# Optimization experiments

Measured on AMD Instinct MI355X. Metric: run time of the kernel, lower is better.

The kernel has to match this reference:

```python
import jax, jax.numpy as jnp
import numpy as np

B, T, N, D, H, NMASK = 8192, 2, 40, 64, 1, 3
EPS = 1e-5


def setup_inputs() -> dict:
    key = jax.random.key(0)
    ks = jax.random.split(key, 12)
    F = T * N * 2 * D  # flattened feature size fed to BatchNorm1d
    return {
        "x": jax.random.normal(ks[0], (B, N, D), jnp.float32),
        "masker": jax.random.uniform(ks[1], (T, NMASK, N, N), jnp.float32, -0.27, 0.27),  # xavier-like
        "ln_gamma": jnp.ones((N,), jnp.float32),
        "ln_beta": jnp.zeros((N,), jnp.float32),
        "gnn_w": jax.random.normal(ks[2], (1, T, H, 2 * D, D), jnp.float32) * 0.05,
        "gnn_b": jax.random.normal(ks[3], (T, H, N, D), jnp.float32) * 0.05,
        "bn_gamma": jnp.ones((H, F), jnp.float32),
        "bn_beta": jnp.zeros((H, F), jnp.float32),
        "bn_mean": jax.random.normal(ks[4], (H, F), jnp.float32) * 0.1,
        "bn_var": jax.random.uniform(ks[5], (H, F), jnp.float32, 0.5, 1.5),
        "gate_w": jax.random.normal(ks[6], (N * D, N), jnp.float32) * 0.02,
        "gate_b": jnp.zeros((N,), jnp.float32),
    }


def reference(x, masker, ln_gamma, ln_beta, gnn_w, gnn_b, bn_gamma, bn_beta, bn_mean, bn_var, gate_w, gate_b):
    b = x.shape[0]
    # broadcast input to towers: (B, T, N, D)
    h = jnp.broadcast_to(x[:, None], (b, T, N, D))
    # adjacency from product of mask matrices: (T, N, N)
    adj = jax.nn.relu(jnp.prod(masker, axis=1))
    mask = (adj != 0).astype(x.dtype)
    # LayerNorm(num_fields) applied on transposed adj == normalize over rows (axis -2)
    mu = adj.mean(axis=-2, keepdims=True)
    var = adj.var(axis=-2, keepdims=True)
    ln = (adj - mu) / jnp.sqrt(var + EPS) * ln_gamma[:, None] + ln_beta[:, None]
    x_masked = ln + (1.0 - mask) * (-1e9) + jnp.eye(N, dtype=x.dtype)
    # softmax over rows (dim=1 of (T,N,N)) then re-mask
    A = jax.nn.softmax(x_masked, axis=1) * mask  # (T, N, N)
    for idx in range(H):
        # nei[b,t,n,d] = sum_m h[b,t,m,d] * A[t,m,n]
        nei = jnp.einsum('btmd,tmn->btnd', h, A)
        hc = jnp.concatenate([h, nei], axis=-1)  # (B,T,N,2D)
        flat = hc.reshape(b, -1)
        flat = (flat - bn_mean[idx]) / jnp.sqrt(bn_var[idx] + EPS) * bn_gamma[idx] + bn_beta[idx]
        hc = flat.reshape(b, T, N, 2 * D)
        # per-tower transform: (B,T,N,2D) x (T,2D,D) -> (B,T,N,D)
        h = jnp.einsum('btnf,tfd->btnd', hc, gnn_w[0, :, idx]) + gnn_b[:, idx]
    # attention pooling over fields
    logits = h.reshape(b, T, N * D) @ gate_w + gate_b  # (B,T,N)
    w = jax.nn.softmax(logits, axis=2)
    return jnp.sum(h * w[..., None], axis=2)  # (B, T, D)
```

## Files before the change

### kernel.cpp

```cpp
#include <hip/hip_runtime.h>
#include <hip/hip_bf16.h>
#include <stdint.h>

typedef float v4f __attribute__((ext_vector_type(4)));
typedef short v8s __attribute__((ext_vector_type(8)));

#define NB 40

__device__ __forceinline__ unsigned short f2b(float f) {
  __hip_bfloat16 h = __float2bfloat16(f);
  unsigned short u;
  __builtin_memcpy(&u, &h, 2);
  return u;
}
__device__ __forceinline__ unsigned pk2(float lo, float hi) {
  __hip_bfloat162 h = __float22bfloat162_rn(make_float2(lo, hi));
  unsigned u;
  __builtin_memcpy(&u, &h, 4);
  return u;
}
__device__ __forceinline__ float b2f16(unsigned short h) {
  return __uint_as_float(((unsigned)h) << 16);
}
__device__ __forceinline__ float blo(unsigned u) { return __uint_as_float(u << 16); }
__device__ __forceinline__ float bhi(unsigned u) { return __uint_as_float(u & 0xFFFF0000u); }


__global__ __launch_bounds__(256) void prep(
    const float* __restrict__ x, const float* __restrict__ masker,
    const float* __restrict__ ln_gamma, const float* __restrict__ ln_beta,
    const float* __restrict__ gnn_w, const float* __restrict__ gnn_b,
    const float* __restrict__ bn_gamma, const float* __restrict__ bn_beta,
    const float* __restrict__ bn_mean, const float* __restrict__ bn_var,
    const float* __restrict__ gate_w,
    unsigned short* __restrict__ A1pk, unsigned short* __restrict__ W2pk,
    unsigned short* __restrict__ Gpk, float* __restrict__ s1,
    float* __restrict__ sNT, float* __restrict__ bias2T,
    unsigned short* __restrict__ xk, unsigned short* __restrict__ xb16)
{
  __shared__ float AtL[2 * NB * NB];
  const int tid = threadIdx.x;

  {
    const int lane = tid & 63, bq = tid >> 6;
    const int b = blockIdx.x * 4 + bq;
    const float* xb = x + (size_t)b * 2560 + lane;
    unsigned u[20];
    #pragma unroll
    for (int mp = 0; mp < 20; ++mp)
      u[mp] = pk2(xb[(2*mp)*64], xb[(2*mp+1)*64]);
    unsigned short* dst = xk + ((size_t)b * 64 + lane) * 40;
    #pragma unroll
    for (int i = 0; i < 5; ++i)
      *(uint4*)(dst + i*8) = make_uint4(u[4*i], u[4*i+1], u[4*i+2], u[4*i+3]);
    const float4* xs4 = (const float4*)(x + (size_t)blockIdx.x * 10240);
    uint2* xd2 = (uint2*)(xb16 + (size_t)blockIdx.x * 10240);
    #pragma unroll
    for (int it = 0; it < 10; ++it) {
      float4 v = xs4[it*256 + tid];
      xd2[it*256 + tid] = make_uint2(pk2(v.x, v.y), pk2(v.z, v.w));
    }
  }

  if (blockIdx.x < 40) {
    const int gid = blockIdx.x * 256 + tid, gsz = 40 * 256;
    for (int e = gid; e < 16384; e += gsz) {
      int frag = e >> 9, rem = e & 511, lane = rem >> 3, jj = rem & 7;
      int t = frag >> 4, ks = (frag >> 2) & 3, dt = frag & 3;
      int f = ks*32 + (lane >> 4)*8 + jj, d = dt*16 + (lane & 15);
      W2pk[e] = f2b(gnn_w[t*8192 + f*64 + d]);
    }
    for (int e = gid; e < 122880; e += gsz) {
      int frag = e >> 9, rem = e & 511, lane = rem >> 3, jj = rem & 7;
      int kt = frag / 3, jt = frag % 3;
      int fl = kt*32 + (lane >> 4)*8 + jj, j = jt*16 + (lane & 15);
      Gpk[e] = f2b(j < NB ? gate_w[fl*NB + j] : 0.f);
    }
    for (int e = gid; e < 5120; e += gsz) {
      int t = e / 2560, n = (e % 2560) / 64, d = e & 63;
      int F = (t*NB + n)*128 + d;
      s1[e] = bn_gamma[F] * rsqrtf(bn_var[F] + 1e-5f);
    }
    for (int e = gid; e < 5120; e += gsz) {
      int t = e / 2560, d = (e % 2560) / 40, n = e % 40;
      int F = (t*NB + n)*128 + 64 + d;
      sNT[e] = bn_gamma[F] * rsqrtf(bn_var[F] + 1e-5f);
    }
    for (int e = gid; e < 5120; e += gsz) {
      int t = e / 2560, d = (e % 2560) / 40, n = e % 40;
      float acc = gnn_b[(t*NB + n)*64 + d];
      int Fb = (t*NB + n)*128;
      for (int f = 0; f < 128; ++f) {
        float s = bn_gamma[Fb+f] * rsqrtf(bn_var[Fb+f] + 1e-5f);
        float o = bn_beta[Fb+f] - bn_mean[Fb+f] * s;
        acc += o * gnn_w[t*8192 + f*64 + d];
      }
      bias2T[e] = acc;
    }
  } else if (blockIdx.x == 40) {
    for (int col = tid; col < 2 * NB; col += 256) {
      int t = col / NB, n = col % NB;
      float adj[NB];
      for (int m = 0; m < NB; ++m) {
        float p = masker[((t*3+0)*NB+m)*NB+n]
                * masker[((t*3+1)*NB+m)*NB+n]
                * masker[((t*3+2)*NB+m)*NB+n];
        adj[m] = p > 0.f ? p : 0.f;
      }
      float mu = 0.f;
      for (int m = 0; m < NB; ++m) mu += adj[m];
      mu *= (1.f/NB);
      float var = 0.f;
      for (int m = 0; m < NB; ++m) { float dv = adj[m]-mu; var += dv*dv; }
      var *= (1.f/NB);
      float inv = rsqrtf(var + 1e-5f);
      float xm[NB]; float mx = -3e38f;
      for (int m = 0; m < NB; ++m) {
        float lnv = (adj[m]-mu)*inv*ln_gamma[m] + ln_beta[m];
        float v = lnv + (adj[m] != 0.f ? 0.f : -1e9f) + (m==n ? 1.f : 0.f);
        xm[m] = v; mx = fmaxf(mx, v);
      }
      float ssum = 0.f;
      for (int m = 0; m < NB; ++m) { xm[m] = __expf(xm[m]-mx); ssum += xm[m]; }
      float isum = 1.f/ssum;
      for (int m = 0; m < NB; ++m)
        AtL[(t*NB+n)*NB+m] = (adj[m] != 0.f) ? xm[m]*isum : 0.f;
    }
    __syncthreads();
    for (int e = tid; e < 6144; e += 256) {
      int frag = e >> 9, rem = e & 511, lane = rem >> 3, jj = rem & 7;
      int t = frag / 6, r2 = frag % 6, nt = r2 >> 1, ks = r2 & 1;
      int n = nt*16 + (lane & 15);
      int m = ks*32 + (lane >> 4)*8 + jj;
      A1pk[e] = f2b((n < NB && m < NB) ? AtL[(t*NB+n)*NB+m] : 0.f);
    }
  }
}

__global__ __launch_bounds__(256) void kernelM(
    const unsigned short* __restrict__ xb16, const unsigned short* __restrict__ xk,
    const unsigned short* __restrict__ A1pk, const unsigned short* __restrict__ W2pk,
    const unsigned short* __restrict__ Gpk, const float* __restrict__ s1,
    const float* __restrict__ sNT, const float* __restrict__ bias2T,
    const float* __restrict__ gate_b, float* __restrict__ out)
{
  __shared__ __align__(16) unsigned short hc[160 * 136];
  __shared__ __align__(16) unsigned short hL[4 * 2568];
  __shared__ float pj[16 * 48];
  __shared__ float wgt[4 * NB];

  const int tid = threadIdx.x;
  const int lane = tid & 63;
  const int w = tid >> 6;
  const int l = lane & 15, q = lane >> 4;
  const int b0 = blockIdx.x * 4;
  unsigned* hcU = (unsigned*)hc;

  v8s b1[4][2];
  #pragma unroll
  for (int i = 0; i < 4; ++i)
    #pragma unroll
    for (int ks = 0; ks < 2; ++ks)
      b1[i][ks] = *(const v8s*)(xk + ((size_t)b0*64 + (w*4+i)*16 + l)*40 + ks*32 + q*8);
  v8s a1[2][3][2];
  #pragma unroll
  for (int t = 0; t < 2; ++t)
    #pragma unroll
    for (int nt = 0; nt < 3; ++nt)
      #pragma unroll
      for (int ks = 0; ks < 2; ++ks)
        a1[t][nt][ks] = *(const v8s*)(A1pk + (((t*3+nt)*2+ks) << 9) + lane*8);
  v8s w2[2][4];
  #pragma unroll
  for (int t = 0; t < 2; ++t)
    #pragma unroll
    for (int ks = 0; ks < 4; ++ks)
      w2[t][ks] = *(const v8s*)(W2pk + (((t*4+ks)*4 + w) << 9) + lane*8);

  uint4 xr[5];

  #pragma unroll
  for (int t = 0; t < 2; ++t) {
    #pragma unroll
    for (int it = 0; it < 5; ++it) {
      const int c = it*256 + tid;
      const int row = c >> 3, dp8 = c & 7;
      if (t == 0)
        xr[it] = *(const uint4*)((const unsigned*)xb16 + (size_t)b0*1280 + row*32 + dp8*4);
      const uint4 xv = xr[it];
      const int n = row % NB;
      const float4 sA = *(const float4*)(s1 + (t*NB + n)*64 + dp8*8);
      const float4 sB = *(const float4*)(s1 + (t*NB + n)*64 + dp8*8 + 4);
      uint4 p;
      p.x = pk2(blo(xv.x)*sA.x, bhi(xv.x)*sA.y);
      p.y = pk2(blo(xv.y)*sA.z, bhi(xv.y)*sA.w);
      p.z = pk2(blo(xv.z)*sB.x, bhi(xv.z)*sB.y);
      p.w = pk2(blo(xv.w)*sB.z, bhi(xv.w)*sB.w);
      *(uint4*)(hcU + row*68 + dp8*4) = p;
    }
    #pragma unroll
    for (int i = 0; i < 4; ++i) {
      const int R = (w*4+i)*16 + l;
      const int bb = R >> 6, d = R & 63;
      #pragma unroll
      for (int nt = 0; nt < 3; ++nt) {
        v4f acc = {0.f, 0.f, 0.f, 0.f};
        acc = __builtin_amdgcn_mfma_f32_16x16x32_bf16(a1[t][nt][0], b1[i][0], acc, 0, 0, 0);
        acc = __builtin_amdgcn_mfma_f32_16x16x32_bf16(a1[t][nt][1], b1[i][1], acc, 0, 0, 0);
        const float4 sv = *(const float4*)(sNT + (t*64+d)*40 + nt*16 + q*4);
        #pragma unroll
        for (int r = 0; r < 4; ++r) {
          int n = nt*16 + q*4 + r;
          if (n < NB) hc[(bb*NB + n)*136 + 64 + d] = f2b(acc[r]*sv[r]);
        }
      }
    }
    __syncthreads();
    #pragma unroll
    for (int mt = 0; mt < 10; ++mt) {
      v4f acc = {0.f, 0.f, 0.f, 0.f};
      #pragma unroll
      for (int ks = 0; ks < 4; ++ks) {
        v8s af = *(const v8s*)(hc + (mt*16 + l)*136 + ks*32 + q*8);
        acc = __builtin_amdgcn_mfma_f32_16x16x32_bf16(af, w2[t][ks], acc, 0, 0, 0);
      }
      const int d = w*16 + l;
      const int G = mt*16 + q*4;
      const int bb = G / NB, n0 = G - bb*NB;
      const float4 bv = *(const float4*)(bias2T + (t*64+d)*40 + n0);
      #pragma unroll
      for (int r = 0; r < 4; ++r)
        hL[bb*2568 + (n0+r)*64 + d] = f2b(acc[r] + bv[r]);
    }
    __syncthreads();
    v4f ac0 = {0,0,0,0}, ac1 = {0,0,0,0}, ac2 = {0,0,0,0};
    for (int kt = w; kt < 80; kt += 4) {
      v8s bf = *(const v8s*)(hL + (l & 3)*2568 + kt*32 + q*8);
      v8s g0 = *(const v8s*)(Gpk + ((kt*3+0) << 9) + lane*8);
      v8s g1 = *(const v8s*)(Gpk + ((kt*3+1) << 9) + lane*8);
      v8s g2 = *(const v8s*)(Gpk + ((kt*3+2) << 9) + lane*8);
      ac0 = __builtin_amdgcn_mfma_f32_16x16x32_bf16(g0, bf, ac0, 0, 0, 0);
      ac1 = __builtin_amdgcn_mfma_f32_16x16x32_bf16(g1, bf, ac1, 0, 0, 0);
      ac2 = __builtin_amdgcn_mfma_f32_16x16x32_bf16(g2, bf, ac2, 0, 0, 0);
    }
    if (l < 4) {
      #pragma unroll
      for (int r = 0; r < 4; ++r) {
        pj[(w*4 + l)*48 +  0 + q*4 + r] = ac0[r];
        pj[(w*4 + l)*48 + 16 + q*4 + r] = ac1[r];
        pj[(w*4 + l)*48 + 32 + q*4 + r] = ac2[r];
      }
    }
    __syncthreads();
    if (tid < 32) {
      const int bb = tid >> 3, s = tid & 7;
      float lv[5]; float mx = -3e38f;
      #pragma unroll
      for (int i = 0; i < 5; ++i) {
        int j = s*5 + i;
        float v = gate_b[j];
        #pragma unroll
        for (int ww = 0; ww < 4; ++ww) v += pj[(ww*4 + bb)*48 + j];
        lv[i] = v; mx = fmaxf(mx, v);
      }
      #pragma unroll
      for (int m = 1; m < 8; m <<= 1) mx = fmaxf(mx, __shfl_xor(mx, m));
      float es = 0.f;
      #pragma unroll
      for (int i = 0; i < 5; ++i) { lv[i] = __expf(lv[i] - mx); es += lv[i]; }
      #pragma unroll
      for (int m = 1; m < 8; m <<= 1) es += __shfl_xor(es, m);
      float inv = 1.f / es;
      #pragma unroll
      for (int i = 0; i < 5; ++i) wgt[bb*NB + s*5 + i] = lv[i]*inv;
    }
    __syncthreads();
    {
      float accp = 0.f;
      #pragma unroll 8
      for (int n = 0; n < NB; ++n)
        accp += b2f16(hL[w*2568 + n*64 + lane]) * wgt[w*NB + n];
      out[((size_t)(b0 + w)*2 + t)*64 + lane] = accp;
    }
  }
}

extern "C" void kernel_launch(void* const* d_in, const int* in_sizes, int n_in,
                              void* d_out, int out_size, void* d_ws, size_t ws_size,
                              hipStream_t stream) {
  const float* x        = (const float*)d_in[0];
  const float* masker   = (const float*)d_in[1];
  const float* ln_gamma = (const float*)d_in[2];
  const float* ln_beta  = (const float*)d_in[3];
  const float* gnn_w    = (const float*)d_in[4];
  const float* gnn_b    = (const float*)d_in[5];
  const float* bn_gamma = (const float*)d_in[6];
  const float* bn_beta  = (const float*)d_in[7];
  const float* bn_mean  = (const float*)d_in[8];
  const float* bn_var   = (const float*)d_in[9];
  const float* gate_w   = (const float*)d_in[10];
  const float* gate_b   = (const float*)d_in[11];
  float* out = (float*)d_out;

  char* ws = (char*)d_ws;
  unsigned short* A1pk   = (unsigned short*)(ws + 0);
  unsigned short* W2pk   = (unsigned short*)(ws + 12288);
  unsigned short* Gpk    = (unsigned short*)(ws + 45056);
  float*          s1     = (float*)(ws + 290816);
  float*          sNT    = (float*)(ws + 311296);
  float*          bias2T = (float*)(ws + 331904);
  unsigned short* xk     = (unsigned short*)(ws + 352384);
  unsigned short* xb16   = (unsigned short*)(ws + 42295552);

  prep<<<2048, 256, 0, stream>>>(x, masker, ln_gamma, ln_beta, gnn_w, gnn_b,
                                 bn_gamma, bn_beta, bn_mean, bn_var, gate_w,
                                 A1pk, W2pk, Gpk, s1, sNT, bias2T, xk, xb16);
  kernelM<<<2048, 256, 0, stream>>>(xb16, xk, A1pk, W2pk, Gpk,
                                    s1, sNT, bias2T, gate_b, out);
}
```

Baseline: 264.9 us.

## Offload bias folding to dedicated prep blocks and halve per-block batch in main kernel

After: 346.2 us. +30.7%, slower.

```diff
diff --git a/kernel.cpp b/kernel.cpp
--- a/kernel.cpp
+++ b/kernel.cpp
@@ -38,10 +38,13 @@
     float* __restrict__ sNT, float* __restrict__ bias2T,
     unsigned short* __restrict__ xk, unsigned short* __restrict__ xb16)
 {
-  __shared__ float AtL[2 * NB * NB];
+  __shared__ __align__(16) char smem[53760];
+  float* AtL   = (float*)smem;
+  float* wtile = (float*)smem;
+  float* oL    = (float*)(smem + 33280);
   const int tid = threadIdx.x;
 
-  {
+  if (blockIdx.x < 2048) {
     const int lane = tid & 63, bq = tid >> 6;
     const int b = blockIdx.x * 4 + bq;
     const float* xb = x + (size_t)b * 2560 + lane;
@@ -85,17 +88,6 @@
       int t = e / 2560, d = (e % 2560) / 40, n = e % 40;
       int F = (t*NB + n)*128 + 64 + d;
       sNT[e] = bn_gamma[F] * rsqrtf(bn_var[F] + 1e-5f);
-    }
-    for (int e = gid; e < 5120; e += gsz) {
-      int t = e / 2560, d = (e % 2560) / 40, n = e % 40;
-      float acc = gnn_b[(t*NB + n)*64 + d];
-      int Fb = (t*NB + n)*128;
-      for (int f = 0; f < 128; ++f) {
-        float s = bn_gamma[Fb+f] * rsqrtf(bn_var[Fb+f] + 1e-5f);
-        float o = bn_beta[Fb+f] - bn_mean[Fb+f] * s;
-        acc += o * gnn_w[t*8192 + f*64 + d];
-      }
-      bias2T[e] = acc;
     }
   } else if (blockIdx.x == 40) {
     for (int col = tid; col < 2 * NB; col += 256) {
@@ -134,34 +126,53 @@
       int m = ks*32 + (lane >> 4)*8 + jj;
       A1pk[e] = f2b((n < NB && m < NB) ? AtL[(t*NB+n)*NB+m] : 0.f);
     }
+  } else if (blockIdx.x >= 2048) {
+    const int t = blockIdx.x - 2048;
+    for (int e = tid; e < 5120; e += 256) {
+      int idx = t*5120 + e;
+      float s = bn_gamma[idx] * rsqrtf(bn_var[idx] + 1e-5f);
+      oL[e] = bn_beta[idx] - bn_mean[idx] * s;
+    }
+    for (int e = tid; e < 8192; e += 256)
+      wtile[(e >> 6)*65 + (e & 63)] = gnn_w[t*8192 + e];
+    __syncthreads();
+    const int d = tid & 63, g = tid >> 6;
+    for (int i = 0; i < 10; ++i) {
+      const int n = g*10 + i;
+      float acc = gnn_b[(t*NB + n)*64 + d];
+      #pragma unroll 8
+      for (int f = 0; f < 128; ++f)
+        acc += oL[n*128 + f] * wtile[f*65 + d];
+      bias2T[(t*64 + d)*40 + n] = acc;
+    }
   }
 }
 
-__global__ __launch_bounds__(256) void kernelM(
+__global__ __launch_bounds__(256, 4) void kernelM(
     const unsigned short* __restrict__ xb16, const unsigned short* __restrict__ xk,
     const unsigned short* __restrict__ A1pk, const unsigned short* __restrict__ W2pk,
     const unsigned short* __restrict__ Gpk, const float* __restrict__ s1,
     const float* __restrict__ sNT, const float* __restrict__ bias2T,
     const float* __restrict__ gate_b, float* __restrict__ out)
 {
-  __shared__ __align__(16) unsigned short hc[160 * 136];
-  __shared__ __align__(16) unsigned short hL[4 * 2568];
+  __shared__ __align__(16) unsigned short hc[80 * 136];
+  __shared__ __align__(16) unsigned short hL[2 * 2568];
   __shared__ float pj[16 * 48];
-  __shared__ float wgt[4 * NB];
+  __shared__ float wgt[2 * NB];
 
   const int tid = threadIdx.x;
   const int lane = tid & 63;
   const int w = tid >> 6;
   const int l = lane & 15, q = lane >> 4;
-  const int b0 = blockIdx.x * 4;
+  const int b0 = blockIdx.x * 2;
   unsigned* hcU = (unsigned*)hc;
 
-  v8s b1[4][2];
+  v8s b1[2][2];
   #pragma unroll
-  for (int i = 0; i < 4; ++i)
+  for (int i = 0; i < 2; ++i)
     #pragma unroll
     for (int ks = 0; ks < 2; ++ks)
-      b1[i][ks] = *(const v8s*)(xk + ((size_t)b0*64 + (w*4+i)*16 + l)*40 + ks*32 + q*8);
+      b1[i][ks] = *(const v8s*)(xk + ((size_t)b0*64 + (w*2+i)*16 + l)*40 + ks*32 + q*8);
   v8s a1[2][3][2];
   #pragma unroll
   for (int t = 0; t < 2; ++t)
@@ -177,30 +188,32 @@
     for (int ks = 0; ks < 4; ++ks)
       w2[t][ks] = *(const v8s*)(W2pk + (((t*4+ks)*4 + w) << 9) + lane*8);
 
-  uint4 xr[5];
+  uint4 xr[3];
 
   #pragma unroll
   for (int t = 0; t < 2; ++t) {
     #pragma unroll
-    for (int it = 0; it < 5; ++it) {
+    for (int it = 0; it < 3; ++it) {
       const int c = it*256 + tid;
-      const int row = c >> 3, dp8 = c & 7;
-      if (t == 0)
-        xr[it] = *(const uint4*)((const unsigned*)xb16 + (size_t)b0*1280 + row*32 + dp8*4);
-      const uint4 xv = xr[it];
-      const int n = row % NB;
-      const float4 sA = *(const float4*)(s1 + (t*NB + n)*64 + dp8*8);
-      const float4 sB = *(const float4*)(s1 + (t*NB + n)*64 + dp8*8 + 4);
-      uint4 p;
-      p.x = pk2(blo(xv.x)*sA.x, bhi(xv.x)*sA.y);
-      p.y = pk2(blo(xv.y)*sA.z, bhi(xv.y)*sA.w);
-      p.z = pk2(blo(xv.z)*sB.x, bhi(xv.z)*sB.y);
-      p.w = pk2(blo(xv.w)*sB.z, bhi(xv.w)*sB.w);
-      *(uint4*)(hcU + row*68 + dp8*4) = p;
-    }
-    #pragma unroll
-    for (int i = 0; i < 4; ++i) {
-      const int R = (w*4+i)*16 + l;
+      if (c < 640) {
+        const int row = c >> 3, dp8 = c & 7;
+        if (t == 0)
+          xr[it] = *(const uint4*)((const unsigned*)xb16 + (size_t)b0*1280 + row*32 + dp8*4);
+        const uint4 xv = xr[it];
+        const int n = row % NB;
+        const float4 sA = *(const float4*)(s1 + (t*NB + n)*64 + dp8*8);
+        const float4 sB = *(const float4*)(s1 + (t*NB + n)*64 + dp8*8 + 4);
+        uint4 p;
+        p.x = pk2(blo(xv.x)*sA.x, bhi(xv.x)*sA.y);
+        p.y = pk2(blo(xv.y)*sA.z, bhi(xv.y)*sA.w);
+        p.z = pk2(blo(xv.z)*sB.x, bhi(xv.z)*sB.y);
+        p.w = pk2(blo(xv.w)*sB.z, bhi(xv.w)*sB.w);
+        *(uint4*)(hcU + row*68 + dp8*4) = p;
+      }
+    }
+    #pragma unroll
+    for (int i = 0; i < 2; ++i) {
+      const int R = (w*2+i)*16 + l;
       const int bb = R >> 6, d = R & 63;
       #pragma unroll
       for (int nt = 0; nt < 3; ++nt) {
@@ -217,7 +230,7 @@
     }
     __syncthreads();
     #pragma unroll
-    for (int mt = 0; mt < 10; ++mt) {
+    for (int mt = 0; mt < 5; ++mt) {
       v4f acc = {0.f, 0.f, 0.f, 0.f};
       #pragma unroll
       for (int ks = 0; ks < 4; ++ks) {
@@ -226,7 +239,7 @@
       }
       const int d = w*16 + l;
       const int G = mt*16 + q*4;
-      const int bb = G / NB, n0 = G - bb*NB;
+      const int bb = (G >= NB) ? 1 : 0, n0 = G - bb*NB;
       const float4 bv = *(const float4*)(bias2T + (t*64+d)*40 + n0);
       #pragma unroll
       for (int r = 0; r < 4; ++r)
@@ -235,7 +248,7 @@
     __syncthreads();
     v4f ac0 = {0,0,0,0}, ac1 = {0,0,0,0}, ac2 = {0,0,0,0};
     for (int kt = w; kt < 80; kt += 4) {
-      v8s bf = *(const v8s*)(hL + (l & 3)*2568 + kt*32 + q*8);
+      v8s bf = *(const v8s*)(hL + (l & 1)*2568 + kt*32 + q*8);
       v8s g0 = *(const v8s*)(Gpk + ((kt*3+0) << 9) + lane*8);
       v8s g1 = *(const v8s*)(Gpk + ((kt*3+1) << 9) + lane*8);
       v8s g2 = *(const v8s*)(Gpk + ((kt*3+2) << 9) + lane*8);
@@ -243,7 +256,7 @@
       ac1 = __builtin_amdgcn_mfma_f32_16x16x32_bf16(g1, bf, ac1, 0, 0, 0);
       ac2 = __builtin_amdgcn_mfma_f32_16x16x32_bf16(g2, bf, ac2, 0, 0, 0);
     }
-    if (l < 4) {
+    if (l < 2) {
       #pragma unroll
       for (int r = 0; r < 4; ++r) {
         pj[(w*4 + l)*48 +  0 + q*4 + r] = ac0[r];
@@ -252,7 +265,7 @@
       }
     }
     __syncthreads();
-    if (tid < 32) {
+    if (tid < 16) {
       const int bb = tid >> 3, s = tid & 7;
       float lv[5]; float mx = -3e38f;
       #pragma unroll
@@ -275,7 +288,7 @@
       for (int i = 0; i < 5; ++i) wgt[bb*NB + s*5 + i] = lv[i]*inv;
     }
     __syncthreads();
-    {
+    if (w < 2) {
       float accp = 0.f;
       #pragma unroll 8
       for (int n = 0; n < NB; ++n)
@@ -312,9 +325,9 @@
   unsigned short* xk     = (unsigned short*)(ws + 352384);
   unsigned short* xb16   = (unsigned short*)(ws + 42295552);
 
-  prep<<<2048, 256, 0, stream>>>(x, masker, ln_gamma, ln_beta, gnn_w, gnn_b,
+  prep<<<2050, 256, 0, stream>>>(x, masker, ln_gamma, ln_beta, gnn_w, gnn_b,
                                  bn_gamma, bn_beta, bn_mean, bn_var, gate_w,
                                  A1pk, W2pk, Gpk, s1, sNT, bias2T, xk, xb16);
-  kernelM<<<2048, 256, 0, stream>>>(xb16, xk, A1pk, W2pk, Gpk,
+  kernelM<<<4096, 256, 0, stream>>>(xb16, xk, A1pk, W2pk, Gpk,
                                     s1, sNT, bias2T, gate_b, out);
 }
```
